# Optimization experiments

Measured on AMD Instinct MI355X. Metric: run time of the kernel, lower is better.

## Reference

```python
import jax, jax.numpy as jnp
import numpy as np

N = 4096      # batch size
D = 512       # flattened feature dim
C = 128       # num classes / output dim
K = 2         # knn k (module default)
ALPHA = 0.0005


def _safe_sqrt(d2):
    # sqrt with zero (not nan) gradient at exactly 0, matching torch.norm
    d2 = jnp.maximum(d2, 0.0)
    safe = jnp.where(d2 > 0, d2, 1.0)
    return jnp.where(d2 > 0, jnp.sqrt(safe), 0.0)


def _pairwise_dist(a):
    # a: [n, d] -> [n, n] euclidean distances via gram trick
    sq = jnp.sum(a * a, axis=1)
    d2 = sq[:, None] + sq[None, :] - 2.0 * (a @ a.T)
    return _safe_sqrt(d2)


def setup_inputs() -> dict:
    key = jax.random.key(0)
    k1, k2, k3, k4 = jax.random.split(key, 4)
    x_batch = jax.random.normal(k1, (N, D), jnp.float32)
    y_batch = jax.random.randint(k2, (N,), 0, C)
    y_output = jax.random.normal(k3, (N, C), jnp.float32)
    W = jax.random.normal(k4, (D, C), jnp.float32) * 0.02
    b = jnp.zeros((C,), jnp.float32)
    return {"x_batch": x_batch, "y_batch": y_batch, "y_output": y_output, "W": W, "b": b}


def reference(x_batch, y_batch, y_output, W, b):
    n = x_batch.shape[0]
    # ---- loss_function(net(x_batch), y_batch): linear net + cross entropy ----
    logits = x_batch.reshape(n, -1) @ W + b                     # [n, C]
    logp = jax.nn.log_softmax(logits, axis=-1)
    loss = -jnp.mean(jnp.take_along_axis(logp, y_batch[:, None], axis=1))

    # ---- compute_weights_based_on_knn (vectorized) ----
    dx = _pairwise_dist(x_batch.reshape(n, -1))                 # [n, n]
    order = jnp.argsort(dx, axis=1)                             # sklearn kneighbors order
    d_sorted = jnp.take_along_axis(dx, order, axis=1)           # sorted distances (sklearn d)
    e_d = jnp.exp(-d_sorted)                                    # [n, n]
    nbr = order[:, :K + 1]                                      # [n, K+1] raw indices
    rows = jnp.arange(n)[:, None]
    nbr_mask = jnp.zeros((n, n), jnp.float32).at[rows, nbr].set(1.0)  # j in neighbors[i]
    same = (y_batch[:, None] == y_batch[None, :]).astype(jnp.float32)
    # w_diff = w_int - 0; w_int[i,j] = e_d[i,j] (raw-j index into sorted e_d, as in source)
    w_diff = e_d * nbr_mask * same                              # [n, n]

    # ---- weighted_output: sum_ij ||y_out[i]-y_out[j]|| * w_diff[i,j] ----
    dy = _pairwise_dist(y_output)                               # [n, n]
    reg = jnp.sum(dy * w_diff)

    return loss + ALPHA * reg
```

## Files before the change

kernel.cpp:

```cpp
#include <hip/hip_runtime.h>
#include <math.h>
#include <stdint.h>

#define N 4096
#define D 512
#define C 128
#define ALPHA 0.0005
#define NCOUNT 1056
#define NCE 64
#define NBLK (NCOUNT + NCE)

typedef __bf16 bf16x8 __attribute__((ext_vector_type(8)));
typedef float f32x4 __attribute__((ext_vector_type(4)));

__device__ __forceinline__ void async16(const void* g, void* l) {
    __builtin_amdgcn_global_load_lds(
        reinterpret_cast<const __attribute__((address_space(1))) uint32_t*>(
            reinterpret_cast<uintptr_t>(g)),
        reinterpret_cast<__attribute__((address_space(3))) uint32_t*>(
            reinterpret_cast<uintptr_t>(l)),
        16, 0, 0);
}

__global__ __launch_bounds__(256) void prep_kernel(const float* __restrict__ x,
                                                   float* __restrict__ sq,
                                                   float* __restrict__ dot0,
                                                   __bf16* __restrict__ xb,
                                                   const float* __restrict__ W,
                                                   __bf16* __restrict__ Wtb,
                                                   unsigned* __restrict__ cnt,
                                                   double* __restrict__ dacc,
                                                   unsigned* __restrict__ done) {
    if (blockIdx.x >= N / 4) {
        const int tid = (blockIdx.x - N / 4) * 256 + threadIdx.x;
        const int k = tid >> 7;
        const int n = tid & 127;
        Wtb[(size_t)n * D + k] = (__bf16)W[tid];
        if (blockIdx.x == N / 4 && threadIdx.x == 0) {
            dacc[0] = 0.0; dacc[1] = 0.0; *done = 0u;
        }
        return;
    }
    const int i = blockIdx.x * 4 + (threadIdx.x >> 6);
    const int l = threadIdx.x & 63;
    const float* xp = x + (size_t)i * D + l * 8;
    const float4 v0 = *(const float4*)(xp);
    const float4 v1 = *(const float4*)(xp + 4);
    const float4 u0 = *(const float4*)(x + l * 8);
    const float4 u1 = *(const float4*)(x + l * 8 + 4);
    float s1 = v0.x * v0.x + v0.y * v0.y + v0.z * v0.z + v0.w * v0.w
             + v1.x * v1.x + v1.y * v1.y + v1.z * v1.z + v1.w * v1.w;
    float s2 = v0.x * u0.x + v0.y * u0.y + v0.z * u0.z + v0.w * u0.w
             + v1.x * u1.x + v1.y * u1.y + v1.z * u1.z + v1.w * u1.w;
    bf16x8 o;
    o[0] = (__bf16)v0.x; o[1] = (__bf16)v0.y; o[2] = (__bf16)v0.z; o[3] = (__bf16)v0.w;
    o[4] = (__bf16)v1.x; o[5] = (__bf16)v1.y; o[6] = (__bf16)v1.z; o[7] = (__bf16)v1.w;
    *(bf16x8*)(xb + (size_t)i * D + l * 8) = o;
    for (int off = 32; off; off >>= 1) {
        s1 += __shfl_down(s1, off);
        s2 += __shfl_down(s2, off);
    }
    if (l == 0) { sq[i] = s1; dot0[i] = s2; cnt[i] = 0u; }
}

__global__ __launch_bounds__(256) void fused_mfma(const __bf16* __restrict__ xb,
                                                  const __bf16* __restrict__ Wtb,
                                                  const float* __restrict__ sq,
                                                  const float* __restrict__ dot0,
                                                  const int* __restrict__ y,
                                                  const float* __restrict__ b,
                                                  unsigned* __restrict__ cnt,
                                                  float* __restrict__ lossrow) {
    __shared__ __bf16 Alds[64 * 128];
    __shared__ __bf16 Blds[128 * 128];
    __shared__ float rmax[64][2];
    __shared__ float rsum[64][2];
    const int t = threadIdx.x;
    const int w = t >> 6, l = t & 63;
    const int wy = w >> 1, wx = w & 1;
    const int kg = l >> 4, lr = l & 15;

    const int bid = (int)blockIdx.x;
    const bool isCE = (bid >= NCOUNT);
    int bi, bj;
    bool edge = false;
    const __bf16* Bbase;
    if (isCE) {
        bi = (bid - NCOUNT) * 64;
        bj = 0;
        Bbase = Wtb;
    } else {
        int si = 0, rem = bid;
        while (rem >= 32 - (si >> 1)) { rem -= 32 - (si >> 1); ++si; }
        const int cj = (si >> 1) + rem;
        bi = si * 64;
        bj = cj * 128;
        edge = (rem == 0);
        Bbase = xb + (size_t)bj * D;
    }
    const __bf16* Abase = xb + (size_t)bi * D;

    f32x4 acc[2][4];
    const f32x4 zero = {0.f, 0.f, 0.f, 0.f};
#pragma unroll
    for (int mt = 0; mt < 2; ++mt)
#pragma unroll
        for (int nt = 0; nt < 4; ++nt) acc[mt][nt] = zero;

    for (int kc = 0; kc < D; kc += 128) {
        __syncthreads();
#pragma unroll
        for (int s = 0; s < 4; ++s) {
            const int e = t + 256 * s;
            const int r = e >> 4, c = e & 15;
            const int sc = c ^ (r & 15);
            async16(Abase + (size_t)r * D + kc + sc * 8, (char*)Alds + e * 16);
        }
#pragma unroll
        for (int s = 0; s < 8; ++s) {
            const int e = t + 256 * s;
            const int r = e >> 4, c = e & 15;
            const int sc = c ^ (r & 15);
            async16(Bbase + (size_t)r * D + kc + sc * 8, (char*)Blds + e * 16);
        }
        __syncthreads();
#pragma unroll
        for (int kk = 0; kk < 4; ++kk) {
            bf16x8 av[2], bv[4];
#pragma unroll
            for (int mt = 0; mt < 2; ++mt) {
                const int row = wy * 32 + mt * 16 + lr;
                const int ch = (kk * 4 + kg) ^ (row & 15);
                av[mt] = *(const bf16x8*)(Alds + row * 128 + ch * 8);
            }
#pragma unroll
            for (int nt = 0; nt < 4; ++nt) {
                const int row = wx * 64 + nt * 16 + lr;
                const int ch = (kk * 4 + kg) ^ (row & 15);
                bv[nt] = *(const bf16x8*)(Blds + row * 128 + ch * 8);
            }
#pragma unroll
            for (int mt = 0; mt < 2; ++mt)
#pragma unroll
                for (int nt = 0; nt < 4; ++nt)
                    acc[mt][nt] = __builtin_amdgcn_mfma_f32_16x16x32_bf16(av[mt], bv[nt], acc[mt][nt], 0, 0, 0);
        }
    }

    if (isCE) {
        int jn[4]; float bb[4];
#pragma unroll
        for (int nt = 0; nt < 4; ++nt) { jn[nt] = wx * 64 + nt * 16 + lr; bb[nt] = b[jn[nt]]; }
#pragma unroll
        for (int mt = 0; mt < 2; ++mt)
#pragma unroll
            for (int r = 0; r < 4; ++r) {
                float m = acc[mt][0][r] + bb[0];
#pragma unroll
                for (int nt = 1; nt < 4; ++nt) m = fmaxf(m, acc[mt][nt][r] + bb[nt]);
                m = fmaxf(m, __shfl_xor(m, 1));
                m = fmaxf(m, __shfl_xor(m, 2));
                m = fmaxf(m, __shfl_xor(m, 4));
                m = fmaxf(m, __shfl_xor(m, 8));
                if (lr == 0) rmax[wy * 32 + mt * 16 + kg * 4 + r][wx] = m;
            }
        __syncthreads();
        float mrow[2][4];
#pragma unroll
        for (int mt = 0; mt < 2; ++mt)
#pragma unroll
            for (int r = 0; r < 4; ++r) {
                const int ri = wy * 32 + mt * 16 + kg * 4 + r;
                mrow[mt][r] = fmaxf(rmax[ri][0], rmax[ri][1]);
                float s = 0.f;
#pragma unroll
                for (int nt = 0; nt < 4; ++nt) s += expf(acc[mt][nt][r] + bb[nt] - mrow[mt][r]);
                s += __shfl_xor(s, 1);
                s += __shfl_xor(s, 2);
                s += __shfl_xor(s, 4);
                s += __shfl_xor(s, 8);
                if (lr == 0) rsum[ri][wx] = s;
            }
        __syncthreads();
#pragma unroll
        for (int mt = 0; mt < 2; ++mt)
#pragma unroll
            for (int r = 0; r < 4; ++r) {
                const int ri = wy * 32 + mt * 16 + kg * 4 + r;
                const int i = bi + ri;
                const float s = rsum[ri][0] + rsum[ri][1];
                const int yi = y[i];
#pragma unroll
                for (int nt = 0; nt < 4; ++nt)
                    if (jn[nt] == yi)
                        lossrow[i] = -(acc[mt][nt][r] + bb[nt] - mrow[mt][r] - logf(s));
            }
    } else {
        const float sq0 = sq[0];
        int jn[4]; float sqj[4], thrj[4];
#pragma unroll
        for (int nt = 0; nt < 4; ++nt) {
            jn[nt] = bj + wx * 64 + nt * 16 + lr;
            sqj[nt] = sq[jn[nt]];
            thrj[nt] = sq0 - 2.0f * dot0[jn[nt]];
        }
        unsigned cj[4] = {0u, 0u, 0u, 0u};
#pragma unroll
        for (int mt = 0; mt < 2; ++mt)
#pragma unroll
            for (int r = 0; r < 4; ++r) {
                const int i = bi + wy * 32 + mt * 16 + kg * 4 + r;
                const float thri = sq0 - 2.0f * dot0[i];
                const float sqi = sq[i];
                unsigned ci = 0;
                if (edge) {
#pragma unroll
                    for (int nt = 0; nt < 4; ++nt) {
                        const float d = acc[mt][nt][r];
                        const int j = jn[nt];
                        if (sqj[nt] - 2.0f * d < thri && j != i && j != 0) ++ci;
                    }
                } else {
#pragma unroll
                    for (int nt = 0; nt < 4; ++nt) {
                        const float d = acc[mt][nt][r];
                        if (sqj[nt] - 2.0f * d < thri) ++ci;
                        if (sqi - 2.0f * d < thrj[nt] && i != 0) ++cj[nt];
                    }
                }
                ci += __shfl_xor((int)ci, 1);
                ci += __shfl_xor((int)ci, 2);
                ci += __shfl_xor((int)ci, 4);
                ci += __shfl_xor((int)ci, 8);
                if (lr == 0 && ci) atomicAdd(&cnt[i], ci);
            }
        if (!edge) {
#pragma unroll
            for (int nt = 0; nt < 4; ++nt) {
                unsigned v = cj[nt];
                v += __shfl_xor((int)v, 16);
                v += __shfl_xor((int)v, 32);
                if (l < 16 && v) atomicAdd(&cnt[jn[nt]], v);
            }
        }
    }
}

__global__ __launch_bounds__(256) void reg_kernel(const float* __restrict__ lossrow,
                                                  const unsigned* __restrict__ cnt,
                                                  const int* __restrict__ y,
                                                  const float* __restrict__ Y,
                                                  double* __restrict__ dacc,
                                                  unsigned* __restrict__ done,
                                                  float* __restrict__ out) {
    const int t = threadIdx.x;
    const int i = blockIdx.x * 128 + (t >> 1);
    const int half = t & 1;
    const int y0 = y[0];

    const float4* yr = (const float4*)(Y + (size_t)i * C + half * 64);
    const float4* yz = (const float4*)(Y + half * 64);
    float d2 = 0.f;
#pragma unroll
    for (int c = 0; c < 16; ++c) {
        const float4 a = yr[c];
        const float4 bb = yz[c];
        const float dx = a.x - bb.x, dy = a.y - bb.y, dz = a.z - bb.z, dw = a.w - bb.w;
        d2 += dx * dx + dy * dy + dz * dz + dw * dw;
    }
    d2 += __shfl_xor(d2, 1);

    double ls = 0.0, rs = 0.0;
    if (half == 0) {
        ls = (double)lossrow[i];
        if (i > 0 && y[i] == y0 && cnt[i] <= 1u)
            rs = sqrt((double)fmaxf(d2, 0.f));
    }
    for (int o = 32; o; o >>= 1) {
        ls += __shfl_down(ls, o);
        rs += __shfl_down(rs, o);
    }
    __shared__ double dl[4], dr[4];
    if ((t & 63) == 0) { dl[t >> 6] = ls; dr[t >> 6] = rs; }
    __syncthreads();
    if (t == 0) {
        atomicAdd(&dacc[0], dl[0] + dl[1] + dl[2] + dl[3]);
        atomicAdd(&dacc[1], dr[0] + dr[1] + dr[2] + dr[3]);
        __threadfence();
        if (atomicAdd(done, 1u) == 31u) {
            const double L = atomicAdd(&dacc[0], 0.0);
            const double R = atomicAdd(&dacc[1], 0.0);
            out[0] = (float)(L / (double)N + ALPHA * R);
        }
    }
}

extern "C" void kernel_launch(void* const* d_in, const int* in_sizes, int n_in,
                              void* d_out, int out_size, void* d_ws, size_t ws_size,
                              hipStream_t stream) {
    const float* x  = (const float*)d_in[0];
    const int*   y  = (const int*)d_in[1];
    const float* Y  = (const float*)d_in[2];
    const float* W  = (const float*)d_in[3];
    const float* b  = (const float*)d_in[4];
    float* out = (float*)d_out;

    float* wsf      = (float*)d_ws;
    float* lossrow  = wsf;
    float* sq       = wsf + N;
    float* dot0     = wsf + 2 * N;
    unsigned* cnt   = (unsigned*)(wsf + 3 * N);
    __bf16* xb      = (__bf16*)(wsf + 4 * N);
    __bf16* Wtb     = (__bf16*)((char*)xb + (size_t)N * D * 2);
    double* dacc    = (double*)((char*)Wtb + (size_t)C * D * 2);
    unsigned* done  = (unsigned*)(dacc + 2);

    prep_kernel<<<N / 4 + 256, 256, 0, stream>>>(x, sq, dot0, xb, W, Wtb, cnt, dacc, done);
    fused_mfma<<<NBLK, 256, 0, stream>>>(xb, Wtb, sq, dot0, y, b, cnt, lossrow);
    reg_kernel<<<32, 256, 0, stream>>>(lossrow, cnt, y, Y, dacc, done, out);
}
```

Before: 101.9 us.

## Restructure fused GEMM into single-wave 64x64 symmetric tiles with register-staged loads

Replaces the 256-thread fused MFMA kernel (64x128 tiles, async global-to-LDS loads, 128-wide K chunks) with single-wavefront blocks computing 64x64 upper-triangular tiles of the Gram matrix. Diagonal tiles load only one operand, and the CE path uses 16-row tiles over all 128 classes. Operands are prefetched into registers for the next 64-wide K chunk while the current one is computed, so no block barriers are needed. Row counts use ballot/popcount instead of shuffle reductions. The aim is more, smaller blocks for better occupancy and no __syncthreads, at the cost of lower per-block data reuse and more register pressure.

```diff
diff --git a/kernel.cpp b/kernel.cpp
--- a/kernel.cpp
+++ b/kernel.cpp
@@ -6,21 +6,13 @@
 #define D 512
 #define C 128
 #define ALPHA 0.0005
-#define NCOUNT 1056
-#define NCE 64
-#define NBLK (NCOUNT + NCE)
+#define NTI 64
+#define NCNT (NTI * (NTI + 1) / 2)
+#define NCE2 (N / 16)
+#define NBLK2 (NCNT + NCE2)
 
 typedef __bf16 bf16x8 __attribute__((ext_vector_type(8)));
 typedef float f32x4 __attribute__((ext_vector_type(4)));
-
-__device__ __forceinline__ void async16(const void* g, void* l) {
-    __builtin_amdgcn_global_load_lds(
-        reinterpret_cast<const __attribute__((address_space(1))) uint32_t*>(
-            reinterpret_cast<uintptr_t>(g)),
-        reinterpret_cast<__attribute__((address_space(3))) uint32_t*>(
-            reinterpret_cast<uintptr_t>(l)),
-        16, 0, 0);
-}
 
 __global__ __launch_bounds__(256) void prep_kernel(const float* __restrict__ x,
                                                    float* __restrict__ sq,
@@ -63,185 +55,217 @@
     if (l == 0) { sq[i] = s1; dot0[i] = s2; cnt[i] = 0u; }
 }
 
-__global__ __launch_bounds__(256) void fused_mfma(const __bf16* __restrict__ xb,
-                                                  const __bf16* __restrict__ Wtb,
-                                                  const float* __restrict__ sq,
-                                                  const float* __restrict__ dot0,
-                                                  const int* __restrict__ y,
-                                                  const float* __restrict__ b,
-                                                  unsigned* __restrict__ cnt,
-                                                  float* __restrict__ lossrow) {
-    __shared__ __bf16 Alds[64 * 128];
-    __shared__ __bf16 Blds[128 * 128];
-    __shared__ float rmax[64][2];
-    __shared__ float rsum[64][2];
-    const int t = threadIdx.x;
-    const int w = t >> 6, l = t & 63;
-    const int wy = w >> 1, wx = w & 1;
-    const int kg = l >> 4, lr = l & 15;
-
+__global__ __launch_bounds__(64) void fused_mfma(const __bf16* __restrict__ xb,
+                                                 const __bf16* __restrict__ Wtb,
+                                                 const float* __restrict__ sq,
+                                                 const float* __restrict__ dot0,
+                                                 const int* __restrict__ y,
+                                                 const float* __restrict__ b,
+                                                 unsigned* __restrict__ cnt,
+                                                 float* __restrict__ lossrow) {
+    __shared__ __bf16 lds[9216];
+    const int l = threadIdx.x;
     const int bid = (int)blockIdx.x;
-    const bool isCE = (bid >= NCOUNT);
-    int bi, bj;
-    bool edge = false;
-    const __bf16* Bbase;
-    if (isCE) {
-        bi = (bid - NCOUNT) * 64;
-        bj = 0;
-        Bbase = Wtb;
-    } else {
-        int si = 0, rem = bid;
-        while (rem >= 32 - (si >> 1)) { rem -= 32 - (si >> 1); ++si; }
-        const int cj = (si >> 1) + rem;
-        bi = si * 64;
-        bj = cj * 128;
-        edge = (rem == 0);
-        Bbase = xb + (size_t)bj * D;
-    }
-    const __bf16* Abase = xb + (size_t)bi * D;
-
-    f32x4 acc[2][4];
-    const f32x4 zero = {0.f, 0.f, 0.f, 0.f};
-#pragma unroll
-    for (int mt = 0; mt < 2; ++mt)
-#pragma unroll
-        for (int nt = 0; nt < 4; ++nt) acc[mt][nt] = zero;
-
-    for (int kc = 0; kc < D; kc += 128) {
-        __syncthreads();
-#pragma unroll
-        for (int s = 0; s < 4; ++s) {
-            const int e = t + 256 * s;
-            const int r = e >> 4, c = e & 15;
-            const int sc = c ^ (r & 15);
-            async16(Abase + (size_t)r * D + kc + sc * 8, (char*)Alds + e * 16);
-        }
+    const int lr = l & 15, kgrp = l >> 4;
+
+    if (bid < NCNT) {
+        int tj = (int)((sqrtf(8.f * (float)bid + 1.f) - 1.f) * 0.5f);
+        while (tj * (tj + 1) / 2 > bid) --tj;
+        while ((tj + 1) * (tj + 2) / 2 <= bid) ++tj;
+        const int ti = bid - tj * (tj + 1) / 2;
+        const int bi = ti * 64, bj = tj * 64;
+        const bool diag = (ti == tj);
+        const __bf16* Ab = xb + (size_t)bi * D;
+        const __bf16* Bb = xb + (size_t)bj * D;
+
+        f32x4 acc[4][4];
+        const f32x4 zero = {0.f, 0.f, 0.f, 0.f};
+#pragma unroll
+        for (int mt = 0; mt < 4; ++mt)
+#pragma unroll
+            for (int nt = 0; nt < 4; ++nt) acc[mt][nt] = zero;
+
+        const int sr = l >> 3;
+        const int scc = l & 7;
+
+        uint4 ra[8], rb[8];
 #pragma unroll
         for (int s = 0; s < 8; ++s) {
-            const int e = t + 256 * s;
-            const int r = e >> 4, c = e & 15;
-            const int sc = c ^ (r & 15);
-            async16(Bbase + (size_t)r * D + kc + sc * 8, (char*)Blds + e * 16);
-        }
-        __syncthreads();
-#pragma unroll
-        for (int kk = 0; kk < 4; ++kk) {
-            bf16x8 av[2], bv[4];
-#pragma unroll
-            for (int mt = 0; mt < 2; ++mt) {
-                const int row = wy * 32 + mt * 16 + lr;
-                const int ch = (kk * 4 + kg) ^ (row & 15);
-                av[mt] = *(const bf16x8*)(Alds + row * 128 + ch * 8);
-            }
-#pragma unroll
-            for (int nt = 0; nt < 4; ++nt) {
-                const int row = wx * 64 + nt * 16 + lr;
-                const int ch = (kk * 4 + kg) ^ (row & 15);
-                bv[nt] = *(const bf16x8*)(Blds + row * 128 + ch * 8);
-            }
-#pragma unroll
-            for (int mt = 0; mt < 2; ++mt)
-#pragma unroll
-                for (int nt = 0; nt < 4; ++nt)
-                    acc[mt][nt] = __builtin_amdgcn_mfma_f32_16x16x32_bf16(av[mt], bv[nt], acc[mt][nt], 0, 0, 0);
-        }
-    }
-
-    if (isCE) {
-        int jn[4]; float bb[4];
-#pragma unroll
-        for (int nt = 0; nt < 4; ++nt) { jn[nt] = wx * 64 + nt * 16 + lr; bb[nt] = b[jn[nt]]; }
-#pragma unroll
-        for (int mt = 0; mt < 2; ++mt)
-#pragma unroll
-            for (int r = 0; r < 4; ++r) {
-                float m = acc[mt][0][r] + bb[0];
-#pragma unroll
-                for (int nt = 1; nt < 4; ++nt) m = fmaxf(m, acc[mt][nt][r] + bb[nt]);
-                m = fmaxf(m, __shfl_xor(m, 1));
-                m = fmaxf(m, __shfl_xor(m, 2));
-                m = fmaxf(m, __shfl_xor(m, 4));
-                m = fmaxf(m, __shfl_xor(m, 8));
-                if (lr == 0) rmax[wy * 32 + mt * 16 + kg * 4 + r][wx] = m;
-            }
-        __syncthreads();
-        float mrow[2][4];
-#pragma unroll
-        for (int mt = 0; mt < 2; ++mt)
-#pragma unroll
-            for (int r = 0; r < 4; ++r) {
-                const int ri = wy * 32 + mt * 16 + kg * 4 + r;
-                mrow[mt][r] = fmaxf(rmax[ri][0], rmax[ri][1]);
-                float s = 0.f;
-#pragma unroll
-                for (int nt = 0; nt < 4; ++nt) s += expf(acc[mt][nt][r] + bb[nt] - mrow[mt][r]);
-                s += __shfl_xor(s, 1);
-                s += __shfl_xor(s, 2);
-                s += __shfl_xor(s, 4);
-                s += __shfl_xor(s, 8);
-                if (lr == 0) rsum[ri][wx] = s;
-            }
-        __syncthreads();
-#pragma unroll
-        for (int mt = 0; mt < 2; ++mt)
-#pragma unroll
-            for (int r = 0; r < 4; ++r) {
-                const int ri = wy * 32 + mt * 16 + kg * 4 + r;
-                const int i = bi + ri;
-                const float s = rsum[ri][0] + rsum[ri][1];
-                const int yi = y[i];
-#pragma unroll
-                for (int nt = 0; nt < 4; ++nt)
-                    if (jn[nt] == yi)
-                        lossrow[i] = -(acc[mt][nt][r] + bb[nt] - mrow[mt][r] - logf(s));
-            }
-    } else {
+            const int r = sr + 8 * s;
+            ra[s] = *(const uint4*)(Ab + (size_t)r * D + scc * 8);
+            if (!diag) rb[s] = *(const uint4*)(Bb + (size_t)r * D + scc * 8);
+        }
+
+        for (int kc = 0;;) {
+#pragma unroll
+            for (int s = 0; s < 8; ++s) {
+                const int r = sr + 8 * s;
+                const int slot = (scc + 2 * ((r >> 2) & 3)) & 7;
+                *(uint4*)(lds + r * 64 + slot * 8) = ra[s];
+                if (!diag) *(uint4*)(lds + 4096 + r * 64 + slot * 8) = rb[s];
+            }
+            const int kn = kc + 64;
+            if (kn < D) {
+#pragma unroll
+                for (int s = 0; s < 8; ++s) {
+                    const int r = sr + 8 * s;
+                    ra[s] = *(const uint4*)(Ab + (size_t)r * D + kn + scc * 8);
+                    if (!diag) rb[s] = *(const uint4*)(Bb + (size_t)r * D + kn + scc * 8);
+                }
+            }
+            const __bf16* Bl = diag ? lds : (lds + 4096);
+#pragma unroll
+            for (int kk = 0; kk < 2; ++kk) {
+                const int ch = kk * 4 + kgrp;
+                bf16x8 av[4], bv[4];
+#pragma unroll
+                for (int mt = 0; mt < 4; ++mt) {
+                    const int r = mt * 16 + lr;
+                    const int slot = (ch + 2 * ((r >> 2) & 3)) & 7;
+                    av[mt] = *(const bf16x8*)(lds + r * 64 + slot * 8);
+                }
+#pragma unroll
+                for (int nt = 0; nt < 4; ++nt) {
+                    const int r = nt * 16 + lr;
+                    const int slot = (ch + 2 * ((r >> 2) & 3)) & 7;
+                    bv[nt] = *(const bf16x8*)(Bl + r * 64 + slot * 8);
+                }
+#pragma unroll
+                for (int mt = 0; mt < 4; ++mt)
+#pragma unroll
+                    for (int nt = 0; nt < 4; ++nt)
+                        acc[mt][nt] = __builtin_amdgcn_mfma_f32_16x16x32_bf16(av[mt], bv[nt], acc[mt][nt], 0, 0, 0);
+            }
+            kc = kn;
+            if (kc >= D) break;
+        }
+
         const float sq0 = sq[0];
         int jn[4]; float sqj[4], thrj[4];
 #pragma unroll
         for (int nt = 0; nt < 4; ++nt) {
-            jn[nt] = bj + wx * 64 + nt * 16 + lr;
+            jn[nt] = bj + nt * 16 + lr;
             sqj[nt] = sq[jn[nt]];
             thrj[nt] = sq0 - 2.0f * dot0[jn[nt]];
         }
-        unsigned cj[4] = {0u, 0u, 0u, 0u};
-#pragma unroll
-        for (int mt = 0; mt < 2; ++mt)
-#pragma unroll
-            for (int r = 0; r < 4; ++r) {
-                const int i = bi + wy * 32 + mt * 16 + kg * 4 + r;
+        unsigned colc[4] = {0u, 0u, 0u, 0u};
+#pragma unroll
+        for (int mt = 0; mt < 4; ++mt)
+#pragma unroll
+            for (int reg = 0; reg < 4; ++reg) {
+                const int i = bi + mt * 16 + kgrp * 4 + reg;
                 const float thri = sq0 - 2.0f * dot0[i];
                 const float sqi = sq[i];
-                unsigned ci = 0;
-                if (edge) {
-#pragma unroll
-                    for (int nt = 0; nt < 4; ++nt) {
-                        const float d = acc[mt][nt][r];
-                        const int j = jn[nt];
-                        if (sqj[nt] - 2.0f * d < thri && j != i && j != 0) ++ci;
+                unsigned v = 0;
+#pragma unroll
+                for (int nt = 0; nt < 4; ++nt) {
+                    const float d = acc[mt][nt][reg];
+                    bool c;
+                    if (diag) {
+                        c = (sqj[nt] - 2.0f * d < thri) && (jn[nt] != i) && (jn[nt] != 0);
+                    } else {
+                        c = (sqj[nt] - 2.0f * d < thri);
+                        if (sqi - 2.0f * d < thrj[nt] && i != 0) ++colc[nt];
                     }
-                } else {
-#pragma unroll
-                    for (int nt = 0; nt < 4; ++nt) {
-                        const float d = acc[mt][nt][r];
-                        if (sqj[nt] - 2.0f * d < thri) ++ci;
-                        if (sqi - 2.0f * d < thrj[nt] && i != 0) ++cj[nt];
-                    }
-                }
-                ci += __shfl_xor((int)ci, 1);
-                ci += __shfl_xor((int)ci, 2);
-                ci += __shfl_xor((int)ci, 4);
-                ci += __shfl_xor((int)ci, 8);
-                if (lr == 0 && ci) atomicAdd(&cnt[i], ci);
-            }
-        if (!edge) {
+                    const unsigned long long m = __ballot(c);
+                    v += (unsigned)__popcll((m >> (16 * kgrp)) & 0xffffULL);
+                }
+                if (lr == 0 && v) atomicAdd(&cnt[i], v);
+            }
+        if (!diag) {
 #pragma unroll
             for (int nt = 0; nt < 4; ++nt) {
-                unsigned v = cj[nt];
-                v += __shfl_xor((int)v, 16);
-                v += __shfl_xor((int)v, 32);
-                if (l < 16 && v) atomicAdd(&cnt[jn[nt]], v);
-            }
+                int v = (int)colc[nt];
+                v += __shfl_xor(v, 16);
+                v += __shfl_xor(v, 32);
+                if (l < 16 && v) atomicAdd(&cnt[jn[nt]], (unsigned)v);
+            }
+        }
+    } else {
+        const int bi = (bid - NCNT) * 16;
+        const __bf16* Ab = xb + (size_t)bi * D;
+
+        f32x4 acc[8];
+        const f32x4 zero = {0.f, 0.f, 0.f, 0.f};
+#pragma unroll
+        for (int nt = 0; nt < 8; ++nt) acc[nt] = zero;
+
+        const int sr = l >> 3;
+        const int scc = l & 7;
+
+        uint4 rca[2], rcb[16];
+#pragma unroll
+        for (int s = 0; s < 2; ++s)
+            rca[s] = *(const uint4*)(Ab + (size_t)(sr + 8 * s) * D + scc * 8);
+#pragma unroll
+        for (int s = 0; s < 16; ++s)
+            rcb[s] = *(const uint4*)(Wtb + (size_t)(sr + 8 * s) * D + scc * 8);
+
+        for (int kc = 0;;) {
+#pragma unroll
+            for (int s = 0; s < 2; ++s) {
+                const int r = sr + 8 * s;
+                const int slot = (scc + 2 * ((r >> 2) & 3)) & 7;
+                *(uint4*)(lds + r * 64 + slot * 8) = rca[s];
+            }
+#pragma unroll
+            for (int s = 0; s < 16; ++s) {
+                const int r = sr + 8 * s;
+                const int slot = (scc + 2 * ((r >> 2) & 3)) & 7;
+                *(uint4*)(lds + 1024 + r * 64 + slot * 8) = rcb[s];
+            }
+            const int kn = kc + 64;
+            if (kn < D) {
+#pragma unroll
+                for (int s = 0; s < 2; ++s)
+                    rca[s] = *(const uint4*)(Ab + (size_t)(sr + 8 * s) * D + kn + scc * 8);
+#pragma unroll
+                for (int s = 0; s < 16; ++s)
+                    rcb[s] = *(const uint4*)(Wtb + (size_t)(sr + 8 * s) * D + kn + scc * 8);
+            }
+#pragma unroll
+            for (int kk = 0; kk < 2; ++kk) {
+                const int ch = kk * 4 + kgrp;
+                const int rA = lr;
+                const int slotA = (ch + 2 * ((rA >> 2) & 3)) & 7;
+                const bf16x8 av = *(const bf16x8*)(lds + rA * 64 + slotA * 8);
+#pragma unroll
+                for (int nt = 0; nt < 8; ++nt) {
+                    const int r = nt * 16 + lr;
+                    const int slot = (ch + 2 * ((r >> 2) & 3)) & 7;
+                    const bf16x8 bv = *(const bf16x8*)(lds + 1024 + r * 64 + slot * 8);
+                    acc[nt] = __builtin_amdgcn_mfma_f32_16x16x32_bf16(av, bv, acc[nt], 0, 0, 0);
+                }
+            }
+            kc = kn;
+            if (kc >= D) break;
+        }
+
+        float bb[8];
+#pragma unroll
+        for (int nt = 0; nt < 8; ++nt) bb[nt] = b[nt * 16 + lr];
+#pragma unroll
+        for (int reg = 0; reg < 4; ++reg) {
+            const int i = bi + kgrp * 4 + reg;
+            float m = acc[0][reg] + bb[0];
+#pragma unroll
+            for (int nt = 1; nt < 8; ++nt) m = fmaxf(m, acc[nt][reg] + bb[nt]);
+            m = fmaxf(m, __shfl_xor(m, 1));
+            m = fmaxf(m, __shfl_xor(m, 2));
+            m = fmaxf(m, __shfl_xor(m, 4));
+            m = fmaxf(m, __shfl_xor(m, 8));
+            float s = 0.f;
+#pragma unroll
+            for (int nt = 0; nt < 8; ++nt) s += expf(acc[nt][reg] + bb[nt] - m);
+            s += __shfl_xor(s, 1);
+            s += __shfl_xor(s, 2);
+            s += __shfl_xor(s, 4);
+            s += __shfl_xor(s, 8);
+            const int yi = y[i];
+#pragma unroll
+            for (int nt = 0; nt < 8; ++nt)
+                if (nt * 16 + lr == yi)
+                    lossrow[i] = -(acc[nt][reg] + bb[nt] - m - logf(s));
         }
     }
 }
@@ -316,6 +340,6 @@
     unsigned* done  = (unsigned*)(dacc + 2);
 
     prep_kernel<<<N / 4 + 256, 256, 0, stream>>>(x, sq, dot0, xb, W, Wtb, cnt, dacc, done);
-    fused_mfma<<<NBLK, 256, 0, stream>>>(xb, Wtb, sq, dot0, y, b, cnt, lossrow);
+    fused_mfma<<<NBLK2, 64, 0, stream>>>(xb, Wtb, sq, dot0, y, b, cnt, lossrow);
     reg_kernel<<<32, 256, 0, stream>>>(lossrow, cnt, y, Y, dacc, done, out);
 }
```

New measurement: 219.5 us. 2.15x slower.
